# Performance work log

Hardware: AMD Instinct MI355X
Metric: run time of the kernel (lower is better)

The kernel has to match this reference:

```python
import jax, jax.numpy as jnp
import numpy as np
import math

B, C, H, W = 4, 256, 56, 56
RC = 32  # max(256 // 8, 8)
EPS = 1e-5


def _conv(x, w, pad):
    return jax.lax.conv_general_dilated(
        x, w, window_strides=(1, 1), padding=[(pad, pad), (pad, pad)],
        dimension_numbers=('NCHW', 'OIHW', 'NCHW'))


def setup_inputs() -> dict:
    key = jax.random.key(0)
    ks = jax.random.split(key, 9)
    s = 0.05  # keep attention logits in a sane range
    return {
        'x': jax.random.normal(ks[0], (B, C, H, W), jnp.float32),
        'wq1': jax.random.normal(ks[1], (RC, C, 1, 1), jnp.float32) * s,
        'wq3': jax.random.normal(ks[2], (RC, C, 3, 3), jnp.float32) * s,
        'wq5': jax.random.normal(ks[3], (RC, C, 5, 5), jnp.float32) * s,
        'wq7': jax.random.normal(ks[4], (RC, C, 7, 7), jnp.float32) * s,
        'wk': jax.random.normal(ks[5], (RC, C, 1, 1), jnp.float32) * s,
        'wv': jax.random.normal(ks[6], (C, C, 1, 1), jnp.float32) * s,
        'wproj': jax.random.normal(ks[7], (C, 4 * C, 1, 1), jnp.float32) * s,
        'gamma': jnp.ones((C,), jnp.float32),
        'beta': jnp.zeros((C,), jnp.float32),
    }


def reference(x, wq1, wq3, wq5, wq7, wk, wv, wproj, gamma, beta):
    b, c, h, w = x.shape
    hw = h * w
    scale = 1.0 / math.sqrt(RC)
    k = _conv(x, wk, 0).reshape(b, RC, hw)   # [B, RC, HW]
    v = _conv(x, wv, 0).reshape(b, c, hw)    # [B, C, HW]
    attended = []
    for wq, pad in ((wq1, 0), (wq3, 1), (wq5, 2), (wq7, 3)):
        q = _conv(x, wq, pad).reshape(b, RC, hw)          # [B, RC, HW]
        scores = jnp.einsum('bri,brj->bij', q, k) * scale  # [B, HW, HW]
        attn = jax.nn.softmax(scores, axis=-1)
        att = jnp.einsum('bcj,bij->bci', v, attn)          # [B, C, HW]
        attended.append(att.reshape(b, c, h, w))
    concat = jnp.concatenate(attended, axis=1)             # [B, 4C, H, W]
    out = _conv(concat, wproj, 0) + x                      # residual before BN
    # BatchNorm2d in training mode: batch stats (biased var), affine
    mean = out.mean(axis=(0, 2, 3), keepdims=True)
    var = out.var(axis=(0, 2, 3), keepdims=True)
    out = (out - mean) * jax.lax.rsqrt(var + EPS)
    return out * gamma[None, :, None, None] + beta[None, :, None, None]
```

## Files before the change

### kernel.cpp

```cpp
#include <hip/hip_runtime.h>
#include <hip/hip_bf16.h>
#include <math.h>

#define HW 3136
#define WIDTH 56
#define CC 256
#define BB 4
#define RCH 32
#define NJT (HW / 64)
#define SCLOG2E 0.2550437041556575f

using bf16x8 = __attribute__((ext_vector_type(8))) short;
using f32x4  = __attribute__((ext_vector_type(4))) float;

static __device__ __forceinline__ unsigned short f2bf(float f) {
    __hip_bfloat16 h = __float2bfloat16(f);
    return *reinterpret_cast<unsigned short*>(&h);
}

__global__ __launch_bounds__(256) void prep_weights(
    const float* __restrict__ wq3, const float* __restrict__ wq5,
    const float* __restrict__ wq7, const float* __restrict__ wproj,
    const float* __restrict__ wk, const float* __restrict__ wq1,
    const float* __restrict__ wv,
    unsigned short* __restrict__ Wb3, unsigned short* __restrict__ Wb5,
    unsigned short* __restrict__ Wb7, unsigned short* __restrict__ Wpb,
    unsigned short* __restrict__ Wkq, unsigned short* __restrict__ Wvb) {
    int e = blockIdx.x * 256 + threadIdx.x;
    if (e < 73728) {
        int c = e & 255, r = (e >> 8) & 31, t = e >> 13;
        Wb3[e] = f2bf(wq3[((size_t)r * 256 + c) * 9 + t]);
    } else if (e < 278528) {
        int i = e - 73728;
        int c = i & 255, r = (i >> 8) & 31, t = i >> 13;
        Wb5[i] = f2bf(wq5[((size_t)r * 256 + c) * 25 + t]);
    } else if (e < 679936) {
        int i = e - 278528;
        int c = i & 255, r = (i >> 8) & 31, t = i >> 13;
        Wb7[i] = f2bf(wq7[((size_t)r * 256 + c) * 49 + t]);
    } else if (e < 942080) {
        int i = e - 679936;
        Wpb[i] = f2bf(wproj[i]);
    } else if (e < 958464) {
        int i = e - 942080;
        Wkq[i] = f2bf(i < 8192 ? wk[i] : wq1[i - 8192]);
    } else if (e < 1024000) {
        int i = e - 958464;
        Wvb[i] = f2bf(wv[i]);
    }
}

__global__ __launch_bounds__(256) void transpose_x(
    const float* __restrict__ x, unsigned short* __restrict__ xT) {
    __shared__ unsigned short tile[32][33];
    const int b = blockIdx.z;
    const int i0 = blockIdx.x * 32, c0 = blockIdx.y * 32;
    const int tx = threadIdx.x & 31, ty = threadIdx.x >> 5;
    #pragma unroll
    for (int k = 0; k < 4; ++k)
        tile[ty + k * 8][tx] = f2bf(x[((size_t)b * CC + c0 + ty + k * 8) * HW + i0 + tx]);
    __syncthreads();
    #pragma unroll
    for (int k = 0; k < 4; ++k)
        xT[((size_t)b * HW + i0 + ty + k * 8) * 256 + c0 + tx] = tile[tx][ty + k * 8];
}

__global__ __launch_bounds__(256) void qk32_mfma(
    const unsigned short* __restrict__ xT, const unsigned short* __restrict__ Wkq,
    unsigned short* __restrict__ Kt, unsigned short* __restrict__ Qt) {
    const int b = blockIdx.y, z = blockIdx.z;
    const int i0 = blockIdx.x * 64;
    const int t = threadIdx.x;
    const int lane = t & 63, w = t >> 6, lg = lane >> 4, li = lane & 15;

    unsigned short* outp = z == 0 ? Kt : Qt;
    const float osc = z == 0 ? 1.0f : SCLOG2E;
    const unsigned short* wb = Wkq + z * 8192;
    const unsigned short* xb = xT + ((size_t)b * HW + i0 + w * 16 + li) * 256;

    const f32x4 z4 = (f32x4){0.f, 0.f, 0.f, 0.f};
    f32x4 acc[2] = {z4, z4};

    for (int c0 = 0; c0 < 256; c0 += 32) {
        bf16x8 ax = *(const bf16x8*)(xb + c0 + lg * 8);
        #pragma unroll
        for (int rs = 0; rs < 2; ++rs) {
            bf16x8 bw = *(const bf16x8*)(wb + (size_t)(rs * 16 + li) * 256 + c0 + lg * 8);
            acc[rs] = __builtin_amdgcn_mfma_f32_16x16x32_bf16(ax, bw, acc[rs], 0, 0, 0);
        }
    }
    unsigned short* qb = outp + ((size_t)b * HW + i0 + w * 16 + lg * 4) * 32;
    #pragma unroll
    for (int rs = 0; rs < 2; ++rs)
        #pragma unroll
        for (int r = 0; r < 4; ++r)
            qb[(size_t)r * 32 + rs * 16 + li] = f2bf(acc[rs][r] * osc);
}

__global__ __launch_bounds__(256) void v_mfma(
    const unsigned short* __restrict__ xT, const unsigned short* __restrict__ Wvb,
    unsigned short* __restrict__ Vb) {
    const int b = blockIdx.y;
    const int i0 = blockIdx.x * 32;
    const int t = threadIdx.x;
    const int lane = t & 63, w = t >> 6, lg = lane >> 4, li = lane & 15;

    const f32x4 z4 = (f32x4){0.f, 0.f, 0.f, 0.f};
    f32x4 acc[4][2];
    #pragma unroll
    for (int ct = 0; ct < 4; ++ct) { acc[ct][0] = z4; acc[ct][1] = z4; }

    const unsigned short* xb = xT + (size_t)b * HW * 256;

    for (int c0 = 0; c0 < 256; c0 += 32) {
        bf16x8 bx[2];
        #pragma unroll
        for (int is = 0; is < 2; ++is)
            bx[is] = *(const bf16x8*)(xb + (size_t)(i0 + is * 16 + li) * 256 + c0 + lg * 8);
        #pragma unroll
        for (int ct = 0; ct < 4; ++ct) {
            bf16x8 aw = *(const bf16x8*)(
                Wvb + (size_t)(w * 64 + ct * 16 + li) * 256 + c0 + lg * 8);
            #pragma unroll
            for (int is = 0; is < 2; ++is)
                acc[ct][is] = __builtin_amdgcn_mfma_f32_16x16x32_bf16(
                    aw, bx[is], acc[ct][is], 0, 0, 0);
        }
    }
    #pragma unroll
    for (int ct = 0; ct < 4; ++ct)
        #pragma unroll
        for (int is = 0; is < 2; ++is)
            #pragma unroll
            for (int r = 0; r < 4; ++r)
                Vb[((size_t)b * CC + w * 64 + ct * 16 + lg * 4 + r) * HW +
                   i0 + is * 16 + li] = f2bf(acc[ct][is][r]);
}

template <int KS>
static __device__ __forceinline__ void qconv_body(
    const unsigned short* __restrict__ xT,
    const unsigned short* __restrict__ Wb,
    unsigned short* __restrict__ q,
    unsigned short (*xs)[40]) {
    constexpr int P = (KS - 1) / 2;
    constexpr int KT = KS * KS;
    constexpr int ROWS = 64 + 114 * P;
    const int b = blockIdx.y;
    const int i0 = blockIdx.x * 64;
    const int t = threadIdx.x;
    const int lane = t & 63;
    const int w = t >> 6;
    const int li = lane & 15;
    const int lg = lane >> 4;

    const int base = i0 - P * 57;
    const int mycol = (i0 + w * 16 + li) % WIDTH;

    f32x4 acc[2];
    acc[0] = (f32x4){0.f, 0.f, 0.f, 0.f};
    acc[1] = (f32x4){0.f, 0.f, 0.f, 0.f};

    const unsigned short* xTb = xT + (size_t)b * HW * 256;

    for (int c0 = 0; c0 < 256; c0 += 32) {
        __syncthreads();
        for (int e = t; e < ROWS * 4; e += 256) {
            int row = e >> 2, cs = e & 3;
            int gidx = base + row;
            uint4 val = make_uint4(0, 0, 0, 0);
            if (gidx >= 0 && gidx < HW)
                val = *(const uint4*)(xTb + (size_t)gidx * 256 + c0 + cs * 8);
            *(uint4*)(&xs[row][cs * 8]) = val;
        }
        __syncthreads();

        #pragma unroll
        for (int tap = 0; tap < KT; ++tap) {
            const int dx = tap % KS - P;
            const int poff = (tap / KS) * WIDTH + tap % KS;
            bf16x8 a = *(const bf16x8*)(&xs[w * 16 + li + poff][lg * 8]);
            if ((unsigned)(mycol + dx) >= (unsigned)WIDTH)
                a = (bf16x8){0, 0, 0, 0, 0, 0, 0, 0};
            const unsigned short* wrow =
                Wb + (size_t)tap * 32 * 256 + c0 + lg * 8;
            bf16x8 b0 = *(const bf16x8*)(wrow + (size_t)li * 256);
            bf16x8 b1 = *(const bf16x8*)(wrow + (size_t)(16 + li) * 256);
            acc[0] = __builtin_amdgcn_mfma_f32_16x16x32_bf16(a, b0, acc[0], 0, 0, 0);
            acc[1] = __builtin_amdgcn_mfma_f32_16x16x32_bf16(a, b1, acc[1], 0, 0, 0);
        }
    }

    unsigned short* qb = q + ((size_t)b * HW + i0 + w * 16 + lg * 4) * 32;
    #pragma unroll
    for (int rs = 0; rs < 2; ++rs)
        #pragma unroll
        for (int r = 0; r < 4; ++r)
            qb[(size_t)r * 32 + rs * 16 + li] = f2bf(acc[rs][r] * SCLOG2E);
}

__global__ __launch_bounds__(256) void qconv_all(
    const unsigned short* __restrict__ xT,
    const unsigned short* __restrict__ Wb3,
    const unsigned short* __restrict__ Wb5,
    const unsigned short* __restrict__ Wb7,
    unsigned short* __restrict__ Qt) {
    __shared__ unsigned short xs[406][40];
    const size_t QSLICE = (size_t)BB * HW * 32;
    if (blockIdx.z == 0)      qconv_body<3>(xT, Wb3, Qt + 1 * QSLICE, xs);
    else if (blockIdx.z == 1) qconv_body<5>(xT, Wb5, Qt + 2 * QSLICE, xs);
    else                      qconv_body<7>(xT, Wb7, Qt + 3 * QSLICE, xs);
}

__global__ __launch_bounds__(256) void flashmfma(
    const unsigned short* __restrict__ Qt, const unsigned short* __restrict__ Kt,
    const unsigned short* __restrict__ Vb, unsigned short* __restrict__ ATTb) {
    const int F = blockIdx.x;
    const int xcd = F & 7;
    const int within = F >> 3;
    const int pair = xcd + 8 * (within / 49);
    const int b = pair & 3;
    const int g = pair >> 2;
    const int i0 = (within % 49) * 64;

    const int t = threadIdx.x;
    const int lane = t & 63;
    const int w = t >> 6;
    const int lg = lane >> 4;
    const int li = lane & 15;

    __shared__ __align__(16) unsigned short Ps[64][72];
    __shared__ float lls[64];

    const bf16x8 aq = *(const bf16x8*)(
        Qt + ((size_t)(g * BB + b) * HW + i0 + w * 16 + li) * 32 + lg * 8);

    const f32x4 z4 = (f32x4){0.f, 0.f, 0.f, 0.f};
    f32x4 acc[4][4];
    #pragma unroll
    for (int ct = 0; ct < 4; ++ct)
        #pragma unroll
        for (int is = 0; is < 4; ++is) acc[ct][is] = z4;

    float lsum[4] = {0.f, 0.f, 0.f, 0.f};

    const unsigned short* Kb = Kt + (size_t)b * HW * 32;
    const unsigned short* Vw = Vb + ((size_t)b * CC + w * 64) * HW;

    for (int jt = 0; jt < NJT; ++jt) {
        const int j0 = jt * 64;

        bf16x8 vf[4][2];
        #pragma unroll
        for (int ct = 0; ct < 4; ++ct) {
            vf[ct][0] = *(const bf16x8*)(
                Vw + (size_t)(ct * 16 + li) * HW + j0 + lg * 8);
            vf[ct][1] = *(const bf16x8*)(
                Vw + (size_t)(ct * 16 + li) * HW + j0 + 32 + lg * 8);
        }

        f32x4 S[4];
        #pragma unroll
        for (int j2 = 0; j2 < 4; ++j2) {
            bf16x8 bk = *(const bf16x8*)(Kb + (size_t)(j0 + j2 * 16 + li) * 32 + lg * 8);
            S[j2] = __builtin_amdgcn_mfma_f32_16x16x32_bf16(aq, bk, z4, 0, 0, 0);
        }

        unsigned int pk0[4], pk1[4];
        #pragma unroll
        for (int r = 0; r < 4; ++r) {
            float p0 = __builtin_amdgcn_exp2f(S[0][r]);
            float p1 = __builtin_amdgcn_exp2f(S[1][r]);
            float p2 = __builtin_amdgcn_exp2f(S[2][r]);
            float p3 = __builtin_amdgcn_exp2f(S[3][r]);
            lsum[r] += (p0 + p1) + (p2 + p3);
            asm("v_cvt_pk_bf16_f32 %0, %1, %2" : "=v"(pk0[r]) : "v"(p0), "v"(p1));
            asm("v_cvt_pk_bf16_f32 %0, %1, %2" : "=v"(pk1[r]) : "v"(p2), "v"(p3));
        }

        __syncthreads();
        #pragma unroll
        for (int r = 0; r < 4; ++r) {
            const int row = w * 16 + lg * 4 + r;
            Ps[row][li]      = (unsigned short)pk0[r];
            Ps[row][16 + li] = (unsigned short)(pk0[r] >> 16);
            Ps[row][32 + li] = (unsigned short)pk1[r];
            Ps[row][48 + li] = (unsigned short)(pk1[r] >> 16);
        }
        __syncthreads();

        bf16x8 bp[4][2];
        #pragma unroll
        for (int is = 0; is < 4; ++is)
            #pragma unroll
            for (int ks = 0; ks < 2; ++ks)
                bp[is][ks] = *(const bf16x8*)(&Ps[is * 16 + li][ks * 32 + lg * 8]);

        __builtin_amdgcn_s_setprio(1);
        #pragma unroll
        for (int ct = 0; ct < 4; ++ct) {
            #pragma unroll
            for (int is = 0; is < 4; ++is) {
                acc[ct][is] = __builtin_amdgcn_mfma_f32_16x16x32_bf16(
                    vf[ct][0], bp[is][0], acc[ct][is], 0, 0, 0);
                acc[ct][is] = __builtin_amdgcn_mfma_f32_16x16x32_bf16(
                    vf[ct][1], bp[is][1], acc[ct][is], 0, 0, 0);
            }
        }
        __builtin_amdgcn_s_setprio(0);
    }

    #pragma unroll
    for (int r = 0; r < 4; ++r) {
        float s = lsum[r];
        #pragma unroll
        for (int off = 1; off < 16; off <<= 1) s += __shfl_xor(s, off);
        if (li == 0) lls[w * 16 + lg * 4 + r] = s;
    }
    __syncthreads();

    float invl[4];
    #pragma unroll
    for (int is = 0; is < 4; ++is) invl[is] = 1.f / lls[is * 16 + li];

    #pragma unroll
    for (int ct = 0; ct < 4; ++ct)
        #pragma unroll
        for (int is = 0; is < 4; ++is)
            #pragma unroll
            for (int r = 0; r < 4; ++r) {
                int c = w * 64 + ct * 16 + lg * 4 + r;
                ATTb[((size_t)b * (4 * CC) + g * CC + c) * HW + i0 + is * 16 + li] =
                    f2bf(acc[ct][is][r] * invl[is]);
            }
}

__global__ __launch_bounds__(256) void gemm_proj(
    const unsigned short* __restrict__ ATTb, const unsigned short* __restrict__ Wpb,
    const float* __restrict__ x, float* __restrict__ out) {
    const int b = blockIdx.y;
    const int i0 = blockIdx.x * 32;
    const int t = threadIdx.x;
    const int lane = t & 63;
    const int w = t >> 6;
    const int lg = lane >> 4;
    const int li = lane & 15;

    __shared__ __align__(16) unsigned short As[32][72];

    const f32x4 z4 = (f32x4){0.f, 0.f, 0.f, 0.f};
    f32x4 acc[4][2];
    #pragma unroll
    for (int ct = 0; ct < 4; ++ct) { acc[ct][0] = z4; acc[ct][1] = z4; }

    for (int k0 = 0; k0 < 1024; k0 += 64) {
        __syncthreads();
        {
            int row = t >> 2, seg = t & 3;
            uint4 v = *(const uint4*)(
                ATTb + ((size_t)b * 1024 + k0 + row) * HW + i0 + seg * 8);
            const unsigned short* sv = (const unsigned short*)&v;
            #pragma unroll
            for (int u = 0; u < 8; ++u) As[seg * 8 + u][row] = sv[u];
        }
        __syncthreads();

        #pragma unroll
        for (int k2 = 0; k2 < 2; ++k2) {
            bf16x8 afr[2];
            #pragma unroll
            for (int is = 0; is < 2; ++is)
                afr[is] = *(const bf16x8*)(&As[is * 16 + li][k2 * 32 + lg * 8]);
            #pragma unroll
            for (int ct = 0; ct < 4; ++ct) {
                bf16x8 wf = *(const bf16x8*)(
                    Wpb + (size_t)(w * 64 + ct * 16 + li) * 1024 + k0 + k2 * 32 + lg * 8);
                #pragma unroll
                for (int is = 0; is < 2; ++is)
                    acc[ct][is] = __builtin_amdgcn_mfma_f32_16x16x32_bf16(
                        wf, afr[is], acc[ct][is], 0, 0, 0);
            }
        }
    }

    #pragma unroll
    for (int ct = 0; ct < 4; ++ct)
        #pragma unroll
        for (int is = 0; is < 2; ++is)
            #pragma unroll
            for (int r = 0; r < 4; ++r) {
                int co = w * 64 + ct * 16 + lg * 4 + r;
                size_t o = ((size_t)b * CC + co) * HW + i0 + is * 16 + li;
                out[o] = acc[ct][is][r] + x[o];
            }
}

__global__ __launch_bounds__(256) void bnstats(
    const float* __restrict__ out, float* __restrict__ mean,
    float* __restrict__ rstd) {
    const int c = blockIdx.x;
    float s = 0.f, s2 = 0.f;
    for (int e = threadIdx.x; e < BB * HW; e += 256) {
        int b = e / HW, i = e - b * HW;
        float v = out[((size_t)b * CC + c) * HW + i];
        s += v; s2 += v * v;
    }
    __shared__ float rs[256], rs2[256];
    rs[threadIdx.x] = s; rs2[threadIdx.x] = s2;
    __syncthreads();
    for (int st = 128; st > 0; st >>= 1) {
        if (threadIdx.x < st) {
            rs[threadIdx.x] += rs[threadIdx.x + st];
            rs2[threadIdx.x] += rs2[threadIdx.x + st];
        }
        __syncthreads();
    }
    if (threadIdx.x == 0) {
        const float n = (float)(BB * HW);
        float m = rs[0] / n;
        float var = rs2[0] / n - m * m;
        mean[c] = m;
        rstd[c] = rsqrtf(var + 1e-5f);
    }
}

__global__ __launch_bounds__(256) void bnapply(
    float* __restrict__ out, const float* __restrict__ mean,
    const float* __restrict__ rstd, const float* __restrict__ gamma,
    const float* __restrict__ beta) {
    size_t idx = (size_t)blockIdx.x * 256 + threadIdx.x;
    if (idx < (size_t)BB * CC * HW) {
        int c = (int)((idx / HW) % CC);
        out[idx] = (out[idx] - mean[c]) * rstd[c] * gamma[c] + beta[c];
    }
}

extern "C" void kernel_launch(void* const* d_in, const int* in_sizes, int n_in,
                              void* d_out, int out_size, void* d_ws, size_t ws_size,
                              hipStream_t stream) {
    const float* x     = (const float*)d_in[0];
    const float* wq1   = (const float*)d_in[1];
    const float* wq3   = (const float*)d_in[2];
    const float* wq5   = (const float*)d_in[3];
    const float* wq7   = (const float*)d_in[4];
    const float* wk    = (const float*)d_in[5];
    const float* wv    = (const float*)d_in[6];
    const float* wproj = (const float*)d_in[7];
    const float* gamma = (const float*)d_in[8];
    const float* beta  = (const float*)d_in[9];
    float* out = (float*)d_out;

    unsigned short* ATTb = (unsigned short*)d_ws;
    unsigned short* Kt   = ATTb + (size_t)BB * 4 * CC * HW;
    unsigned short* Qt   = Kt + (size_t)BB * HW * 32;
    unsigned short* Vb   = Qt + (size_t)4 * BB * HW * 32;
    unsigned short* xT   = Vb + (size_t)BB * CC * HW;
    unsigned short* Wb3  = xT + (size_t)BB * HW * CC;
    unsigned short* Wb5  = Wb3 + (size_t)9 * 32 * 256;
    unsigned short* Wb7  = Wb5 + (size_t)25 * 32 * 256;
    unsigned short* Wpb  = Wb7 + (size_t)49 * 32 * 256;
    unsigned short* Wkq  = Wpb + (size_t)256 * 1024;
    unsigned short* Wvb  = Wkq + (size_t)2 * 32 * 256;
    float* mean = (float*)(Wvb + (size_t)256 * 256);
    float* rstd = mean + CC;

    dim3 blk(256);

    prep_weights<<<dim3(4000), blk, 0, stream>>>(
        wq3, wq5, wq7, wproj, wk, wq1, wv, Wb3, Wb5, Wb7, Wpb, Wkq, Wvb);
    transpose_x<<<dim3(HW / 32, CC / 32, BB), blk, 0, stream>>>(x, xT);

    qk32_mfma<<<dim3(HW / 64, BB, 2), blk, 0, stream>>>(xT, Wkq, Kt, Qt);
    v_mfma<<<dim3(HW / 32, BB), blk, 0, stream>>>(xT, Wvb, Vb);

    qconv_all<<<dim3(HW / 64, BB, 3), blk, 0, stream>>>(xT, Wb3, Wb5, Wb7, Qt);

    flashmfma<<<dim3(8 * 2 * (HW / 64)), blk, 0, stream>>>(Qt, Kt, Vb, ATTb);

    gemm_proj<<<dim3(HW / 32, BB), blk, 0, stream>>>(ATTb, Wpb, x, out);

    bnstats<<<dim3(CC), blk, 0, stream>>>(out, mean, rstd);
    bnapply<<<dim3((BB * CC * HW + 255) / 256), blk, 0, stream>>>(out, mean, rstd, gamma, beta);
}
```

Measured before the change: 484.4 us.

## Store attention output position-major and drop LDS transpose in projection GEMM

The attention kernel now writes its normalized output as [B, HW, 4C] with packed bf16 conversions and 8-byte stores, instead of channel-major scalar stores. The projection GEMM then reads its A fragments straight from global memory along the contiguous channel dimension. This removes the shared-memory staging, the scalar transpose and two barriers per k-step. In exchange the GEMM relies on cache for operand reuse and issues more global loads per MFMA.

```diff
diff --git a/kernel.cpp b/kernel.cpp
--- a/kernel.cpp
+++ b/kernel.cpp
@@ -214,7 +214,7 @@
 
 __global__ __launch_bounds__(256) void flashmfma(
     const unsigned short* __restrict__ Qt, const unsigned short* __restrict__ Kt,
-    const unsigned short* __restrict__ Vb, unsigned short* __restrict__ ATTb) {
+    const unsigned short* __restrict__ Vb, unsigned short* __restrict__ ATTt) {
     const int F = blockIdx.x;
     const int xcd = F & 7;
     const int within = F >> 3;
@@ -326,17 +326,22 @@
     #pragma unroll
     for (int ct = 0; ct < 4; ++ct)
         #pragma unroll
-        for (int is = 0; is < 4; ++is)
-            #pragma unroll
-            for (int r = 0; r < 4; ++r) {
-                int c = w * 64 + ct * 16 + lg * 4 + r;
-                ATTb[((size_t)b * (4 * CC) + g * CC + c) * HW + i0 + is * 16 + li] =
-                    f2bf(acc[ct][is][r] * invl[is]);
-            }
+        for (int is = 0; is < 4; ++is) {
+            float v0 = acc[ct][is][0] * invl[is];
+            float v1 = acc[ct][is][1] * invl[is];
+            float v2 = acc[ct][is][2] * invl[is];
+            float v3 = acc[ct][is][3] * invl[is];
+            unsigned int lo, hi;
+            asm("v_cvt_pk_bf16_f32 %0, %1, %2" : "=v"(lo) : "v"(v0), "v"(v1));
+            asm("v_cvt_pk_bf16_f32 %0, %1, %2" : "=v"(hi) : "v"(v2), "v"(v3));
+            uint2 pk; pk.x = lo; pk.y = hi;
+            *(uint2*)(ATTt + ((size_t)b * HW + i0 + is * 16 + li) * 1024 +
+                      g * 256 + w * 64 + ct * 16 + lg * 4) = pk;
+        }
 }
 
 __global__ __launch_bounds__(256) void gemm_proj(
-    const unsigned short* __restrict__ ATTb, const unsigned short* __restrict__ Wpb,
+    const unsigned short* __restrict__ ATTt, const unsigned short* __restrict__ Wpb,
     const float* __restrict__ x, float* __restrict__ out) {
     const int b = blockIdx.y;
     const int i0 = blockIdx.x * 32;
@@ -346,40 +351,27 @@
     const int lg = lane >> 4;
     const int li = lane & 15;
 
-    __shared__ __align__(16) unsigned short As[32][72];
-
     const f32x4 z4 = (f32x4){0.f, 0.f, 0.f, 0.f};
     f32x4 acc[4][2];
     #pragma unroll
     for (int ct = 0; ct < 4; ++ct) { acc[ct][0] = z4; acc[ct][1] = z4; }
 
-    for (int k0 = 0; k0 < 1024; k0 += 64) {
-        __syncthreads();
-        {
-            int row = t >> 2, seg = t & 3;
-            uint4 v = *(const uint4*)(
-                ATTb + ((size_t)b * 1024 + k0 + row) * HW + i0 + seg * 8);
-            const unsigned short* sv = (const unsigned short*)&v;
-            #pragma unroll
-            for (int u = 0; u < 8; ++u) As[seg * 8 + u][row] = sv[u];
-        }
-        __syncthreads();
-
-        #pragma unroll
-        for (int k2 = 0; k2 < 2; ++k2) {
-            bf16x8 afr[2];
+    const unsigned short* ab = ATTt + (size_t)b * HW * 1024;
+
+    for (int k0 = 0; k0 < 1024; k0 += 32) {
+        bf16x8 afr[2];
+        #pragma unroll
+        for (int is = 0; is < 2; ++is)
+            afr[is] = *(const bf16x8*)(
+                ab + (size_t)(i0 + is * 16 + li) * 1024 + k0 + lg * 8);
+        #pragma unroll
+        for (int ct = 0; ct < 4; ++ct) {
+            bf16x8 wf = *(const bf16x8*)(
+                Wpb + (size_t)(w * 64 + ct * 16 + li) * 1024 + k0 + lg * 8);
             #pragma unroll
             for (int is = 0; is < 2; ++is)
-                afr[is] = *(const bf16x8*)(&As[is * 16 + li][k2 * 32 + lg * 8]);
-            #pragma unroll
-            for (int ct = 0; ct < 4; ++ct) {
-                bf16x8 wf = *(const bf16x8*)(
-                    Wpb + (size_t)(w * 64 + ct * 16 + li) * 1024 + k0 + k2 * 32 + lg * 8);
-                #pragma unroll
-                for (int is = 0; is < 2; ++is)
-                    acc[ct][is] = __builtin_amdgcn_mfma_f32_16x16x32_bf16(
-                        wf, afr[is], acc[ct][is], 0, 0, 0);
-            }
+                acc[ct][is] = __builtin_amdgcn_mfma_f32_16x16x32_bf16(
+                    wf, afr[is], acc[ct][is], 0, 0, 0);
         }
     }
 
@@ -450,8 +442,8 @@
     const float* beta  = (const float*)d_in[9];
     float* out = (float*)d_out;
 
-    unsigned short* ATTb = (unsigned short*)d_ws;
-    unsigned short* Kt   = ATTb + (size_t)BB * 4 * CC * HW;
+    unsigned short* ATTt = (unsigned short*)d_ws;
+    unsigned short* Kt   = ATTt + (size_t)BB * 4 * CC * HW;
     unsigned short* Qt   = Kt + (size_t)BB * HW * 32;
     unsigned short* Vb   = Qt + (size_t)4 * BB * HW * 32;
     unsigned short* xT   = Vb + (size_t)BB * CC * HW;
@@ -475,9 +467,9 @@
 
     qconv_all<<<dim3(HW / 64, BB, 3), blk, 0, stream>>>(xT, Wb3, Wb5, Wb7, Qt);
 
-    flashmfma<<<dim3(8 * 2 * (HW / 64)), blk, 0, stream>>>(Qt, Kt, Vb, ATTb);
-
-    gemm_proj<<<dim3(HW / 32, BB), blk, 0, stream>>>(ATTb, Wpb, x, out);
+    flashmfma<<<dim3(8 * 2 * (HW / 64)), blk, 0, stream>>>(Qt, Kt, Vb, ATTt);
+
+    gemm_proj<<<dim3(HW / 32, BB), blk, 0, stream>>>(ATTt, Wpb, x, out);
 
     bnstats<<<dim3(CC), blk, 0, stream>>>(out, mean, rstd);
     bnapply<<<dim3((BB * CC * HW + 255) / 256), blk, 0, stream>>>(out, mean, rstd, gamma, beta);
```

New measurement: 496.1 us. 2.4% more time.
